# Kernel tuning notes

Hardware: AMD Instinct MI355X
Metric: run time of the kernel (lower is better)

Reference implementation:

```python
import jax, jax.numpy as jnp
import numpy as np

H = 256   # hidden_dim
V = 256   # byte vocab


def _lstm_cell(h, c, gates):
    # PyTorch gate order: i, f, g, o
    i, f, g, o = jnp.split(gates, 4, axis=-1)
    c = jax.nn.sigmoid(f) * c + jax.nn.sigmoid(i) * jnp.tanh(g)
    h = jax.nn.sigmoid(o) * jnp.tanh(c)
    return h, c


def _lstm_layer(x, w_ih, w_hh, b):
    # x: (B, T, In) -> (B, T, H); single direction, zero init state
    B = x.shape[0]
    Hh = w_hh.shape[1]
    xg = jnp.einsum('bti,gi->btg', x, w_ih) + b  # precompute input contribution
    def step(carry, xg_t):
        h, c = carry
        h, c = _lstm_cell(h, c, xg_t + h @ w_hh.T)
        return (h, c), h
    init = (jnp.zeros((B, Hh), x.dtype), jnp.zeros((B, Hh), x.dtype))
    _, hs = jax.lax.scan(step, init, jnp.swapaxes(xg, 0, 1))
    return jnp.swapaxes(hs, 0, 1)


def setup_inputs() -> dict:
    key = jax.random.key(0)
    ks = jax.random.split(key, 16)
    B, T = 256, 512
    s = 0.08
    def rn(k, shape):
        return jax.random.normal(k, shape, jnp.float32) * s
    return dict(
        text_bytes=jax.random.randint(ks[0], (B, T), 0, V),
        max_nefs_len=100,
        emb=rn(ks[1], (V, H)),
        enc_w_ih_l0=rn(ks[2], (2, 4 * H, H)),        # (dir, 4H, in)
        enc_w_hh_l0=rn(ks[3], (2, 4 * H, H)),
        enc_b_l0=rn(ks[4], (2, 4 * H)),              # b_ih + b_hh fused
        enc_w_ih_rest=rn(ks[5], (2, 2, 4 * H, 2 * H)),  # layers 1-2, input=2H
        enc_w_hh_rest=rn(ks[6], (2, 2, 4 * H, H)),
        enc_b_rest=rn(ks[7], (2, 2, 4 * H)),
        dec_w_ih_l0=rn(ks[8], (4 * H, 2 * H)),       # decoder input_size=2H
        dec_w_ih_rest=rn(ks[9], (2, 4 * H, H)),
        dec_w_hh=rn(ks[10], (3, 4 * H, H)),
        dec_b=rn(ks[11], (3, 4 * H)),
        proj_w=rn(ks[12], (256, H)),
        proj_b=rn(ks[13], (256,)),
    )


def reference(text_bytes, max_nefs_len, emb, enc_w_ih_l0, enc_w_hh_l0, enc_b_l0,
              enc_w_ih_rest, enc_w_hh_rest, enc_b_rest, dec_w_ih_l0,
              dec_w_ih_rest, dec_w_hh, dec_b, proj_w, proj_b):
    B = text_bytes.shape[0]
    # --- bidirectional 3-layer encoder ---
    x = emb[text_bytes]  # (B, T, H)
    for l in range(3):
        if l == 0:
            wih, whh, b = enc_w_ih_l0, enc_w_hh_l0, enc_b_l0
        else:
            wih, whh, b = enc_w_ih_rest[l - 1], enc_w_hh_rest[l - 1], enc_b_rest[l - 1]
        fwd = _lstm_layer(x, wih[0], whh[0], b[0])
        rev = jnp.flip(_lstm_layer(jnp.flip(x, 1), wih[1], whh[1], b[1]), 1)
        x = jnp.concatenate([fwd, rev], axis=-1)  # (B, T, 2H)
    enc_out = x

    dec_in0 = enc_out[:, 0, :]  # (B, 2H)
    z = jnp.zeros((3, B, H), enc_out.dtype)

    def dec_step(carry, _):
        h, c, inp = carry
        x_l = inp
        new_h, new_c = [], []
        for l in range(3):
            wih = dec_w_ih_l0 if l == 0 else dec_w_ih_rest[l - 1]
            hl, cl = _lstm_cell(h[l], c[l], x_l @ wih.T + h[l] @ dec_w_hh[l].T + dec_b[l])
            new_h.append(hl)
            new_c.append(cl)
            x_l = hl
        logits = x_l @ proj_w.T + proj_b  # (B, 256)
        nxt = jnp.argmax(logits, axis=-1)
        e = emb[nxt]  # (B, H)
        # NOTE: original torch code feeds a 256-d embedding into the 512-d-input
        # decoder LSTM (runtime error at t=1); zero-pad to 2H to make it well-defined.
        inp_next = jnp.concatenate([e, jnp.zeros_like(e)], axis=-1)
        return (jnp.stack(new_h), jnp.stack(new_c), inp_next), logits

    _, logits_seq = jax.lax.scan(dec_step, (z, z, dec_in0), None, length=int(max_nefs_len))
    return jnp.swapaxes(logits_seq, 0, 1)  # (B, max_nefs_len, 256)
```

## Files before the change

### kernel.cpp

```cpp
#include <hip/hip_runtime.h>
#include <hip/hip_bf16.h>

#define Hh 256
#define G4 1024
#define Bsz 256
#define TN 512
#define LDEC 100

#define OD0 0
#define ODR 524288
#define ODH 1048576
#define OPJ 1835008
#define OEM 1900544

typedef __attribute__((ext_vector_type(4))) float f32x4;
typedef __attribute__((ext_vector_type(8))) short s16x8;
typedef __attribute__((ext_vector_type(8))) unsigned short u16x8;

__device__ __forceinline__ unsigned short bf_hi(float v) {
  __hip_bfloat16 h = __float2bfloat16(v);
  return *(unsigned short*)&h;
}
__device__ __forceinline__ float bf_f(unsigned short u) {
  unsigned int x = ((unsigned int)u) << 16;
  return *(float*)&x;
}
__device__ __forceinline__ float sigm(float x) { return 1.f / (1.f + expf(-x)); }

__global__ void k_fill(float* __restrict__ p, int n, float v) {
  int i = blockIdx.x * 256 + threadIdx.x;
  if (i < n) p[i] = v;
}

__global__ void k_split(const float* __restrict__ src, unsigned short* __restrict__ hi,
                        unsigned short* __restrict__ lo, int n) {
  int i = blockIdx.x * 256 + threadIdx.x;
  if (i < n) {
    float v = src[i];
    unsigned short h = bf_hi(v);
    hi[i] = h;
    lo[i] = bf_hi(v - bf_f(h));
  }
}

__global__ void k_split3(const float* __restrict__ src, unsigned short* __restrict__ p0,
                         unsigned short* __restrict__ p1, unsigned short* __restrict__ p2,
                         int n) {
  int i = blockIdx.x * 256 + threadIdx.x;
  if (i < n) {
    float v = src[i];
    unsigned short a = bf_hi(v);
    float r1 = v - bf_f(a);
    unsigned short b = bf_hi(r1);
    float r2 = r1 - bf_f(b);
    p0[i] = a;
    p1[i] = b;
    p2[i] = bf_hi(r2);
  }
}

__global__ __launch_bounds__(256) void k_gemm(
    const short* __restrict__ X, const int* __restrict__ text,
    const unsigned short* __restrict__ eh, const unsigned short* __restrict__ el, int l0,
    int K,
    const unsigned short* __restrict__ wh_, const unsigned short* __restrict__ wl_, int wstride,
    const float* __restrict__ bias, float* __restrict__ xg, int s0, int both) {
  int mt = blockIdx.x, nt = blockIdx.y, z = blockIdx.z;
  int slot, dir, w;
  if (both) { slot = z; dir = z & 1; w = z >> 1; }
  else      { slot = z * 2 + 1; dir = 1; w = z; }
  int s = s0 + w;
  int t = dir ? (TN - 1 - s) : s;
  const unsigned short* wh = wh_ + (size_t)dir * wstride;
  const unsigned short* wl = wl_ + (size_t)dir * wstride;
  const float* bp = bias + dir * G4;
  __shared__ unsigned short Ah[64][40], Al[64][40], Bh[128][40], Bl[128][40];
  int tid = threadIdx.x, wave = tid >> 6, lane = tid & 63;
  f32x4 acc[8];
#pragma unroll
  for (int i = 0; i < 8; ++i) acc[i] = (f32x4){0.f, 0.f, 0.f, 0.f};

  int ar = tid >> 2, akq = (tid & 3) * 8;
  int brow = mt * 64 + ar;
  const unsigned short *aeh = nullptr, *ael = nullptr;
  const short* ax = nullptr;
  if (l0) {
    int tok = text[brow * TN + t];
    aeh = eh + tok * 256 + akq;
    ael = el + tok * 256 + akq;
  } else {
    ax = X + ((size_t)brow * TN + t) * 512 + akq;
  }
  int br = tid >> 1, bkq = (tid & 1) * 16;
  int g = nt * 128 + br;
  const unsigned short* bsrch = wh + (size_t)g * K + bkq;
  const unsigned short* bsrcl = wl + (size_t)g * K + bkq;

  for (int kk = 0; kk < K; kk += 32) {
    __syncthreads();
    if (l0) {
      *(u16x8*)&Ah[ar][akq] = *(const u16x8*)(aeh + kk);
      *(u16x8*)&Al[ar][akq] = *(const u16x8*)(ael + kk);
    } else {
      s16x8 sv = *(const s16x8*)(ax + kk);
      u16x8 hv, lv;
#pragma unroll
      for (int j = 0; j < 8; ++j) {
        float a = (float)sv[j] * (1.f / 32767.f);
        unsigned short h = bf_hi(a);
        hv[j] = h;
        lv[j] = bf_hi(a - bf_f(h));
      }
      *(u16x8*)&Ah[ar][akq] = hv;
      *(u16x8*)&Al[ar][akq] = lv;
    }
    *(u16x8*)&Bh[br][bkq]      = *(const u16x8*)(bsrch + kk);
    *(u16x8*)&Bh[br][bkq + 8]  = *(const u16x8*)(bsrch + kk + 8);
    *(u16x8*)&Bl[br][bkq]      = *(const u16x8*)(bsrcl + kk);
    *(u16x8*)&Bl[br][bkq + 8]  = *(const u16x8*)(bsrcl + kk + 8);
    __syncthreads();

    int m = wave * 16 + (lane & 15);
    int kq = (lane >> 4) * 8;
    s16x8 ah = *(s16x8*)&Ah[m][kq];
    s16x8 al = *(s16x8*)&Al[m][kq];
#pragma unroll
    for (int nf = 0; nf < 8; ++nf) {
      s16x8 bh = *(s16x8*)&Bh[nf * 16 + (lane & 15)][kq];
      s16x8 bl = *(s16x8*)&Bl[nf * 16 + (lane & 15)][kq];
      acc[nf] = __builtin_amdgcn_mfma_f32_16x16x32_bf16(ah, bh, acc[nf], 0, 0, 0);
      acc[nf] = __builtin_amdgcn_mfma_f32_16x16x32_bf16(al, bh, acc[nf], 0, 0, 0);
      acc[nf] = __builtin_amdgcn_mfma_f32_16x16x32_bf16(ah, bl, acc[nf], 0, 0, 0);
    }
  }
  int col = lane & 15, rq = (lane >> 4) * 4;
  float* outp = xg + (size_t)slot * 262144;
#pragma unroll
  for (int nf = 0; nf < 8; ++nf) {
    int gg = nt * 128 + nf * 16 + col;
    float bv = bp[gg];
#pragma unroll
    for (int r = 0; r < 4; ++r) {
      int b = mt * 64 + wave * 16 + rq + r;
      outp[(size_t)b * 1024 + gg] = acc[nf][r] + bv;
    }
  }
}

#define MF6(ACC, P0, P1, P2, WO)                                                         \
  {                                                                                      \
    s16x8 bf0 = *(const s16x8*)&(P0)[WO];                                                \
    s16x8 bf1 = *(const s16x8*)&(P1)[WO];                                                \
    s16x8 bf2 = *(const s16x8*)&(P2)[WO];                                                \
    ACC = __builtin_amdgcn_mfma_f32_16x16x32_bf16(a1, bf1, ACC, 0, 0, 0);                \
    ACC = __builtin_amdgcn_mfma_f32_16x16x32_bf16(a0, bf2, ACC, 0, 0, 0);                \
    ACC = __builtin_amdgcn_mfma_f32_16x16x32_bf16(a2, bf0, ACC, 0, 0, 0);                \
    ACC = __builtin_amdgcn_mfma_f32_16x16x32_bf16(a1, bf0, ACC, 0, 0, 0);                \
    ACC = __builtin_amdgcn_mfma_f32_16x16x32_bf16(a0, bf1, ACC, 0, 0, 0);                \
    ACC = __builtin_amdgcn_mfma_f32_16x16x32_bf16(a0, bf0, ACC, 0, 0, 0);                \
  }

#define MFMA_BF16 __builtin_amdgcn_mfma_f32_16x16x32_bf16

__global__ __launch_bounds__(512) void k_wstep(
    const float* __restrict__ xg,
    const unsigned short* __restrict__ w0, const unsigned short* __restrict__ w1,
    const unsigned short* __restrict__ w2,
    unsigned short* __restrict__ Hg,
    float* __restrict__ Cst,
    short* __restrict__ X, short* __restrict__ Sf, short* __restrict__ Sr,
    float* __restrict__ dec_in, int* __restrict__ bar, int s0, int W, int mode) {
  int jt = blockIdx.x, bs = blockIdx.y, dir = blockIdx.z;
  if (mode == 2 && dir == 0 && s0 != 0) return;
  int nsteps = (mode == 2 && dir == 0) ? 1 : W;
  int j16 = jt * 16;
  int b0 = bs * 128;
  const unsigned short* wp0 = w0 + dir * 262144;
  const unsigned short* wp1 = w1 + dir * 262144;
  const unsigned short* wp2 = w2 + dir * 262144;
  int* gbase = bar + ((dir * 2 + bs) * 16) * 32;
  int* slot = gbase + jt * 32;

  __shared__ unsigned short Wl[3][4][16][256];
  int tid = threadIdx.x, lane = tid & 63, wv = tid >> 6;
  int m15 = lane & 15, lq = lane >> 4, hk8 = lq * 8, r0 = lq * 4;

  for (int v = tid; v < 6144; v += 512) {
    int pl = v / 2048;
    int rem = v - pl * 2048;
    int gq = rem >> 9;
    int r = (rem >> 5) & 15;
    int c = rem & 31;
    const unsigned short* wp = (pl == 0) ? wp0 : ((pl == 1) ? wp1 : wp2);
    *(u16x8*)&Wl[pl][gq][r][(c ^ (r & 7)) * 8] =
        *(const u16x8*)&wp[((size_t)(gq * 256 + j16 + r)) * 256 + c * 8];
  }
  f32x4 cx;
  if (s0 == 0) {
    cx = (f32x4){0.f, 0.f, 0.f, 0.f};
  } else {
#pragma unroll
    for (int r = 0; r < 4; ++r)
      cx[r] = Cst[(size_t)dir * 65536 + (b0 + wv * 16 + r0 + r) * 256 + j16 + m15];
  }
  __syncthreads();

  int j = j16 + m15;
  for (int w = 0; w < nsteps; ++w) {
    int s = s0 + w;
    int p0 = s & 1, p1 = p0 ^ 1;
    const float* xgp = xg + (size_t)(2 * w + dir) * 262144;
    const unsigned short* hr0 = Hg + ((size_t)(dir * 2 + p0) * 3 + 0) * 65536;
    const unsigned short* hr1 = Hg + ((size_t)(dir * 2 + p0) * 3 + 1) * 65536;
    const unsigned short* hr2 = Hg + ((size_t)(dir * 2 + p0) * 3 + 2) * 65536;
    unsigned short* hw0 = Hg + ((size_t)(dir * 2 + p1) * 3 + 0) * 65536;
    unsigned short* hw1 = Hg + ((size_t)(dir * 2 + p1) * 3 + 1) * 65536;
    unsigned short* hw2 = Hg + ((size_t)(dir * 2 + p1) * 3 + 2) * 65536;

    float xv[4][4];
#pragma unroll
    for (int r = 0; r < 4; ++r) {
      const float* xr = xgp + (size_t)(b0 + wv * 16 + r0 + r) * 1024 + j;
      xv[r][0] = xr[0];
      xv[r][1] = xr[256];
      xv[r][2] = xr[512];
      xv[r][3] = xr[768];
    }

    f32x4 acc[4];
#pragma unroll
    for (int gq = 0; gq < 4; ++gq) acc[gq] = (f32x4){0.f, 0.f, 0.f, 0.f};

    size_t hbase = (size_t)(b0 + wv * 16 + m15) * 256 + hk8;
    s16x8 a0 = *(const s16x8*)&hr0[hbase];
    s16x8 a1 = *(const s16x8*)&hr1[hbase];
    s16x8 a2 = *(const s16x8*)&hr2[hbase];
#pragma unroll
    for (int kk = 0; kk < 8; ++kk) {
      s16x8 n0, n1, n2;
      if (kk < 7) {
        n0 = *(const s16x8*)&hr0[hbase + (kk + 1) * 32];
        n1 = *(const s16x8*)&hr1[hbase + (kk + 1) * 32];
        n2 = *(const s16x8*)&hr2[hbase + (kk + 1) * 32];
      }
      int cc = ((kk * 4 + lq) ^ (m15 & 7)) * 8;
#pragma unroll
      for (int gq = 0; gq < 4; ++gq) {
        s16x8 B0 = *(const s16x8*)&Wl[0][gq][m15][cc];
        s16x8 B1 = *(const s16x8*)&Wl[1][gq][m15][cc];
        s16x8 B2 = *(const s16x8*)&Wl[2][gq][m15][cc];
        f32x4 t2 = acc[gq];
        t2 = MFMA_BF16(a1, B1, t2, 0, 0, 0);
        t2 = MFMA_BF16(a0, B2, t2, 0, 0, 0);
        t2 = MFMA_BF16(a2, B0, t2, 0, 0, 0);
        t2 = MFMA_BF16(a1, B0, t2, 0, 0, 0);
        t2 = MFMA_BF16(a0, B1, t2, 0, 0, 0);
        t2 = MFMA_BF16(a0, B0, t2, 0, 0, 0);
        acc[gq] = t2;
      }
      a0 = n0; a1 = n1; a2 = n2;
    }
    int t = dir ? (TN - 1 - s) : s;
#pragma unroll
    for (int r = 0; r < 4; ++r) {
      int brow = b0 + wv * 16 + r0 + r;
      float gi = acc[0][r] + xv[r][0];
      float gf = acc[1][r] + xv[r][1];
      float gg = acc[2][r] + xv[r][2];
      float go = acc[3][r] + xv[r][3];
      float cn = sigm(gf) * cx[r] + sigm(gi) * tanhf(gg);
      float hn = sigm(go) * tanhf(cn);
      cx[r] = cn;
      unsigned short q0v = bf_hi(hn);
      float rr1 = hn - bf_f(q0v);
      unsigned short q1v = bf_hi(rr1);
      unsigned short q2v = bf_hi(rr1 - bf_f(q1v));
      size_t ho = (size_t)brow * 256 + j;
      __builtin_nontemporal_store(q0v, &hw0[ho]);
      __builtin_nontemporal_store(q1v, &hw1[ho]);
      __builtin_nontemporal_store(q2v, &hw2[ho]);
      short q = (short)__float2int_rn(hn * 32767.f);
      if (mode == 0) {
        __builtin_nontemporal_store(q, &X[((size_t)brow * TN + t) * 512 + (dir << 8) + j]);
      } else if (mode == 1) {
        if (dir == 0) {
          if (t >= 256)
            __builtin_nontemporal_store(q, &X[((size_t)brow * TN + t) * 512 + j]);
          else
            __builtin_nontemporal_store(q, &Sf[((size_t)t * 256 + brow) * 256 + j]);
        } else {
          if (t < 256)
            __builtin_nontemporal_store(q, &X[((size_t)brow * TN + t) * 512 + 256 + j]);
          else
            __builtin_nontemporal_store(q, &Sr[((size_t)(t - 256) * 256 + brow) * 256 + j]);
        }
      } else {
        if (t == 0)
          __builtin_nontemporal_store(hn, &dec_in[(size_t)brow * 512 + (dir << 8) + j]);
      }
    }
    if (w < nsteps - 1) {
      __builtin_amdgcn_fence(__ATOMIC_RELEASE, "agent");
      __syncthreads();
      if (tid == 0)
        __hip_atomic_store(slot, s + 1, __ATOMIC_RELAXED, __HIP_MEMORY_SCOPE_AGENT);
      if (tid < 16) {
        while (__hip_atomic_load(gbase + tid * 32, __ATOMIC_RELAXED,
                                 __HIP_MEMORY_SCOPE_AGENT) < s + 1) {}
      }
      __syncthreads();
      __builtin_amdgcn_fence(__ATOMIC_ACQUIRE, "agent");
    }
  }
#pragma unroll
  for (int r = 0; r < 4; ++r)
    Cst[(size_t)dir * 65536 + (b0 + wv * 16 + r0 + r) * 256 + j16 + m15] = cx[r];
}

__global__ void k_flush(short* __restrict__ X, const short* __restrict__ Sf,
                        const short* __restrict__ Sr) {
  int side = blockIdx.y;
  int idx = blockIdx.x * 256 + threadIdx.x;
  int t0 = idx >> 13;
  int b = (idx >> 5) & 255;
  int j0 = (idx & 31) * 8;
  if (side == 0) {
    *(s16x8*)&X[((size_t)b * TN + t0) * 512 + j0] =
        *(const s16x8*)&Sf[((size_t)t0 * 256 + b) * 256 + j0];
  } else {
    int t = 256 + t0;
    *(s16x8*)&X[((size_t)b * TN + t) * 512 + 256 + j0] =
        *(const s16x8*)&Sr[((size_t)t0 * 256 + b) * 256 + j0];
  }
}

#define DWAITA(BASE, TARGET)                                                      \
  __syncthreads();                                                                \
  if (tid < 32) {                                                                 \
    while (__hip_atomic_load((BASE) + tid * 32, __ATOMIC_RELAXED,                 \
                             __HIP_MEMORY_SCOPE_AGENT) < (TARGET)) {}             \
  }                                                                               \
  __syncthreads();                                                                \
  __builtin_amdgcn_fence(__ATOMIC_ACQUIRE, "agent");

#define DPOSTA(BASE, VAL)                                                         \
  __builtin_amdgcn_fence(__ATOMIC_RELEASE, "agent");                              \
  __syncthreads();                                                                \
  if (tid == 0)                                                                   \
    __hip_atomic_store((BASE) + gix * 32, (VAL), __ATOMIC_RELAXED,                \
                       __HIP_MEMORY_SCOPE_AGENT);

#define CMM(MT, CI)                                                               \
  {                                                                               \
    int cs_ = ((CI) ^ (m15 & 7)) * 8;                                             \
    _Pragma("unroll") for (int p = 0; p < 2; ++p) {                               \
      s16x8 B0 = *(const s16x8*)&W[((size_t)(0 * 2 + p) * 16 + m15) * KT + cs_];  \
      s16x8 B1 = *(const s16x8*)&W[((size_t)(1 * 2 + p) * 16 + m15) * KT + cs_];  \
      s16x8 B2 = *(const s16x8*)&W[((size_t)(2 * 2 + p) * 16 + m15) * KT + cs_];  \
      f32x4 t2 = acc[MT][p];                                                      \
      t2 = MFMA_BF16(a1, B1, t2, 0, 0, 0);                                        \
      t2 = MFMA_BF16(a0, B2, t2, 0, 0, 0);                                        \
      t2 = MFMA_BF16(a2, B0, t2, 0, 0, 0);                                        \
      t2 = MFMA_BF16(a1, B0, t2, 0, 0, 0);                                        \
      t2 = MFMA_BF16(a0, B1, t2, 0, 0, 0);                                        \
      t2 = MFMA_BF16(a0, B0, t2, 0, 0, 0);                                        \
      acc[MT][p] = t2;                                                            \
    }                                                                             \
  }

__global__ __launch_bounds__(512) void k_dec2(
    const float* __restrict__ dec_in0,
    const unsigned short* __restrict__ q0, const unsigned short* __restrict__ q1,
    const unsigned short* __restrict__ q2,
    const float* __restrict__ db, const float* __restrict__ pb,
    unsigned short* __restrict__ Dh, int* __restrict__ toksG,
    int* __restrict__ bar, float* __restrict__ out) {
  __shared__ unsigned short W[73728];
  __shared__ float LG[8][256];
  __shared__ float rvv[8][16];
  __shared__ int rii[8][16];
  int tid = threadIdx.x, lane = tid & 63, wv = tid >> 6;
  int m15 = lane & 15, lq = lane >> 4, hk8 = lq * 8;
  int blk = blockIdx.x;
  int grp = blk >> 5;
  int gix = blk & 31;
  int j8 = gix * 8;
  int KT = (grp == 0) ? 768 : 512;
  int* arr0 = bar;
  int* arr1 = bar + 1024;
  int* arr2 = bar + 2048;
  int* arr3 = bar + 3072;

  {
    int KC = KT >> 3;
    int nvec = 6 * 16 * KC;
    for (int v = tid; v < nvec; v += 512) {
      int c = v % KC;
      int r = (v / KC) & 15;
      int pp = v / (KC * 16);
      int pl = pp >> 1, p = pp & 1;
      int g = (2 * p + (r >> 3)) * 256 + j8 + (r & 7);
      int k = c * 8;
      size_t so;
      if (grp == 0)
        so = (k < 512) ? (size_t)OD0 + (size_t)g * 512 + k
                       : (size_t)ODH + (size_t)g * 256 + (k - 512);
      else if (grp == 1)
        so = (k < 256) ? (size_t)ODR + (size_t)g * 256 + k
                       : (size_t)ODH + 262144 + (size_t)g * 256 + (k - 256);
      else
        so = (k < 256) ? (size_t)ODR + 262144 + (size_t)g * 256 + k
                       : (size_t)ODH + 524288 + (size_t)g * 256 + (k - 256);
      const unsigned short* qs = (pl == 0) ? q0 : ((pl == 1) ? q1 : q2);
      int cs = c ^ (r & 7);
      *(u16x8*)&W[((size_t)pp * 16 + r) * KT + (size_t)cs * 8] = *(const u16x8*)&qs[so];
    }
  }
  __syncthreads();

  int cc8 = m15 & 7;
  int jcol = j8 + cc8;
  float bI = db[grp * 1024 + jcol];
  float bF = db[grp * 1024 + 256 + jcol];
  float bG = db[grp * 1024 + 512 + jcol];
  float bO = db[grp * 1024 + 768 + jcol];
  f32x4 cx[2];
  cx[0] = (f32x4){0.f, 0.f, 0.f, 0.f};
  cx[1] = (f32x4){0.f, 0.f, 0.f, 0.f};

  int gb = gix * 8;
  int mrow = m15 & 7;
  int r0q = lq * 4;
  bool act = (r0q < 8);

  for (int t = 0; t < LDEC; ++t) {
    int pw = (t & 1) ^ 1, pr = t & 1;
    if (grp == 0) { DWAITA(arr3, t) }
    else if (grp == 1) { DWAITA(arr0, t + 1) }
    else { DWAITA(arr1, t + 1) }

    f32x4 acc[2][2];
#pragma unroll
    for (int mt = 0; mt < 2; ++mt)
#pragma unroll
      for (int p = 0; p < 2; ++p) acc[mt][p] = (f32x4){0.f, 0.f, 0.f, 0.f};

    if (grp == 0) {
      if (t == 0) {
        for (int kk = 0; kk < 16; ++kk) {
#pragma unroll
          for (int mt = 0; mt < 2; ++mt) {
            int browA = wv * 32 + mt * 16 + m15;
            const float* src = dec_in0 + (size_t)browA * 512 + kk * 32 + hk8;
            s16x8 a0, a1, a2;
#pragma unroll
            for (int e = 0; e < 8; ++e) {
              float v = src[e];
              unsigned short t0 = bf_hi(v);
              float r1 = v - bf_f(t0);
              unsigned short t1 = bf_hi(r1);
              a0[e] = (short)t0; a1[e] = (short)t1; a2[e] = (short)bf_hi(r1 - bf_f(t1));
            }
            CMM(mt, kk * 4 + lq)
          }
        }
      } else {
        for (int kk = 0; kk < 8; ++kk) {
#pragma unroll
          for (int mt = 0; mt < 2; ++mt) {
            int browA = wv * 32 + mt * 16 + m15;
            int tok = toksG[browA];
            size_t eo = (size_t)OEM + (size_t)tok * 256 + kk * 32 + hk8;
            s16x8 a0 = *(const s16x8*)&q0[eo];
            s16x8 a1 = *(const s16x8*)&q1[eo];
            s16x8 a2 = *(const s16x8*)&q2[eo];
            CMM(mt, kk * 4 + lq)
          }
        }
      }
    } else {
      const unsigned short* x0p = Dh + (size_t)(((grp - 1) * 2 + pw) * 3 + 0) * 65536;
      const unsigned short* x1p = Dh + (size_t)(((grp - 1) * 2 + pw) * 3 + 1) * 65536;
      const unsigned short* x2p = Dh + (size_t)(((grp - 1) * 2 + pw) * 3 + 2) * 65536;
      for (int kk = 0; kk < 8; ++kk) {
#pragma unroll
        for (int mt = 0; mt < 2; ++mt) {
          size_t ao = (size_t)(wv * 32 + mt * 16 + m15) * 256 + kk * 32 + hk8;
          s16x8 a0 = *(const s16x8*)&x0p[ao];
          s16x8 a1 = *(const s16x8*)&x1p[ao];
          s16x8 a2 = *(const s16x8*)&x2p[ao];
          CMM(mt, kk * 4 + lq)
        }
      }
    }
    {
      int cb = (grp == 0) ? 64 : 32;
      const unsigned short* h0p = Dh + (size_t)((grp * 2 + pr) * 3 + 0) * 65536;
      const unsigned short* h1p = Dh + (size_t)((grp * 2 + pr) * 3 + 1) * 65536;
      const unsigned short* h2p = Dh + (size_t)((grp * 2 + pr) * 3 + 2) * 65536;
      for (int kk = 0; kk < 8; ++kk) {
#pragma unroll
        for (int mt = 0; mt < 2; ++mt) {
          size_t ao = (size_t)(wv * 32 + mt * 16 + m15) * 256 + kk * 32 + hk8;
          s16x8 a0 = *(const s16x8*)&h0p[ao];
          s16x8 a1 = *(const s16x8*)&h1p[ao];
          s16x8 a2 = *(const s16x8*)&h2p[ao];
          CMM(mt, cb + kk * 4 + lq)
        }
      }
    }
    {
      unsigned short* hw0 = Dh + (size_t)((grp * 2 + pw) * 3 + 0) * 65536;
      unsigned short* hw1 = Dh + (size_t)((grp * 2 + pw) * 3 + 1) * 65536;
      unsigned short* hw2 = Dh + (size_t)((grp * 2 + pw) * 3 + 2) * 65536;
#pragma unroll
      for (int mt = 0; mt < 2; ++mt) {
        f32x4 fx, ox;
#pragma unroll
        for (int e = 0; e < 4; ++e) {
          fx[e] = __shfl_xor(acc[mt][0][e], 8);
          ox[e] = __shfl_xor(acc[mt][1][e], 8);
        }
        if (m15 < 8) {
#pragma unroll
          for (int r = 0; r < 4; ++r) {
            int brow = wv * 32 + mt * 16 + lq * 4 + r;
            float gi = acc[mt][0][r] + bI;
            float gf = fx[r] + bF;
            float gg = acc[mt][1][r] + bG;
            float go = ox[r] + bO;
            float cn = sigm(gf) * cx[mt][r] + sigm(gi) * tanhf(gg);
            float hn = sigm(go) * tanhf(cn);
            cx[mt][r] = cn;
            unsigned short p0v = bf_hi(hn);
            float rr1 = hn - bf_f(p0v);
            unsigned short p1v = bf_hi(rr1);
            unsigned short p2v = bf_hi(rr1 - bf_f(p1v));
            size_t ho = (size_t)brow * 256 + jcol;
            hw0[ho] = p0v; hw1[ho] = p1v; hw2[ho] = p2v;
          }
        }
      }
    }
    if (grp == 0) { DPOSTA(arr0, t + 1) }
    else if (grp == 1) { DPOSTA(arr1, t + 1) }
    else { DPOSTA(arr2, t + 1) }

    if (grp == 2) {
      DWAITA(arr2, t + 1)
      unsigned short* H2 = &W[49152];
      for (int i = tid; i < 6144; i += 512) {
        int pl = i / 2048;
        int rem = i - pl * 2048;
        int row = rem >> 8, col = rem & 255;
        H2[pl * 2112 + row * 264 + col] =
            Dh[(size_t)((2 * 2 + pw) * 3 + pl) * 65536 + (size_t)(gb + row) * 256 + col];
      }
      __syncthreads();
      f32x4 pacc[2];
#pragma unroll
      for (int jj = 0; jj < 2; ++jj) pacc[jj] = (f32x4){0.f, 0.f, 0.f, 0.f};
      for (int kk = 0; kk < 8; ++kk) {
        s16x8 a0 = *(const s16x8*)&H2[0 * 2112 + mrow * 264 + kk * 32 + hk8];
        s16x8 a1 = *(const s16x8*)&H2[1 * 2112 + mrow * 264 + kk * 32 + hk8];
        s16x8 a2 = *(const s16x8*)&H2[2 * 2112 + mrow * 264 + kk * 32 + hk8];
#pragma unroll
        for (int jj = 0; jj < 2; ++jj) {
          int v = wv * 32 + jj * 16 + m15;
          size_t wo = OPJ + (size_t)v * 256 + kk * 32 + hk8;
          MF6(pacc[jj], q0, q1, q2, wo)
        }
      }
      if (act) {
#pragma unroll
        for (int jj = 0; jj < 2; ++jj) {
          int v = wv * 32 + jj * 16 + m15;
          float pbv = pb[v];
#pragma unroll
          for (int r = 0; r < 4; ++r) LG[r0q + r][v] = pacc[jj][r] + pbv;
        }
      }
      __syncthreads();
      for (int i = tid; i < 2048; i += 512) {
        int row = i >> 8, v = i & 255;
        out[((size_t)(gb + row) * LDEC + t) * 256 + v] = LG[row][v];
      }
      if (tid < 128) {
        int prow = tid >> 4, pp = tid & 15;
        float bv = LG[prow][pp * 16];
        int bidx = pp * 16;
        for (int i2 = 1; i2 < 16; ++i2) {
          float v2 = LG[prow][pp * 16 + i2];
          if (v2 > bv) { bv = v2; bidx = pp * 16 + i2; }
        }
        rvv[prow][pp] = bv;
        rii[prow][pp] = bidx;
      }
      __syncthreads();
      if (tid < 8) {
        float best = rvv[tid][0];
        int bi = rii[tid][0];
        for (int qq = 1; qq < 16; ++qq) {
          float v2 = rvv[tid][qq];
          int ii = rii[tid][qq];
          if (v2 > best || (v2 == best && ii < bi)) { best = v2; bi = ii; }
        }
        toksG[gb + tid] = bi;
      }
      DPOSTA(arr3, t + 1)
    }
  }
}

extern "C" void kernel_launch(void* const* d_in, const int* in_sizes, int n_in,
                              void* d_out, int out_size, void* d_ws, size_t ws_size,
                              hipStream_t stream) {
  const int* text = (const int*)d_in[0];
  const float* emb = (const float*)d_in[2];
  const float* w_ih_l0 = (const float*)d_in[3];
  const float* w_hh_l0 = (const float*)d_in[4];
  const float* b_l0 = (const float*)d_in[5];
  const float* w_ih_r = (const float*)d_in[6];
  const float* w_hh_r = (const float*)d_in[7];
  const float* b_r = (const float*)d_in[8];
  const float* dwih0 = (const float*)d_in[9];
  const float* dwihr = (const float*)d_in[10];
  const float* dwhh = (const float*)d_in[11];
  const float* db = (const float*)d_in[12];
  const float* pw = (const float*)d_in[13];
  const float* pb = (const float*)d_in[14];

  char* ws = (char*)d_ws;
  short *X, *Sf, *Sr;
  unsigned short *wihh, *wihl, *whp0, *whp1, *whp2, *embh, *embl, *Hg, *Dh;
  unsigned short *q0, *q1, *q2;
  float *XG, *Cst, *dec_in;
  int *bar, *toksG;
  int W = 0;
  for (int Wv = 8; Wv >= 4 && W == 0; Wv >>= 1) {
    size_t off = 0;
    X    = (short*)(ws + off);          off += (size_t)Bsz * TN * 512 * 2;
    Sf   = (short*)(ws + off);          off += (size_t)256 * Bsz * 256 * 2;
    Sr   = (short*)(ws + off);          off += (size_t)256 * Bsz * 256 * 2;
    XG   = (float*)(ws + off);          off += (size_t)2 * Wv * 262144 * 4;
    wihh = (unsigned short*)(ws + off); off += 2621440ull * 2;
    wihl = (unsigned short*)(ws + off); off += 2621440ull * 2;
    whp0 = (unsigned short*)(ws + off); off += 1572864ull * 2;
    whp1 = (unsigned short*)(ws + off); off += 1572864ull * 2;
    whp2 = (unsigned short*)(ws + off); off += 1572864ull * 2;
    embh = (unsigned short*)(ws + off); off += 65536 * 2;
    embl = (unsigned short*)(ws + off); off += 65536 * 2;
    q0   = (unsigned short*)(ws + off); off += 1966080ull * 2;
    q1   = (unsigned short*)(ws + off); off += 1966080ull * 2;
    q2   = (unsigned short*)(ws + off); off += 1966080ull * 2;
    Hg   = (unsigned short*)(ws + off); off += 786432ull * 2;
    Dh   = (unsigned short*)(ws + off); off += 1179648ull * 2;
    Cst  = (float*)(ws + off);          off += (size_t)2 * Bsz * Hh * 4;
    dec_in = (float*)(ws + off);        off += (size_t)Bsz * 512 * 4;
    toksG = (int*)(ws + off);           off += 1024;
    bar  = (int*)(ws + off);            off += 40960;
    if (ws_size >= off) W = Wv;
  }
  if (W == 0) {
    float dval = 1000.0f + (float)(ws_size >> 20);
    k_fill<<<(out_size + 255) / 256, 256, 0, stream>>>((float*)d_out, out_size, dval);
    return;
  }

  k_fill<<<40, 256, 0, stream>>>((float*)bar, 10240, 0.f);
  k_fill<<<2304, 256, 0, stream>>>((float*)Dh, 589824, 0.f);

  k_split<<<2048, 256, 0, stream>>>(w_ih_l0, wihh, wihl, 524288);
  k_split<<<8192, 256, 0, stream>>>(w_ih_r, wihh + 524288, wihl + 524288, 2097152);
  k_split<<<256, 256, 0, stream>>>(emb, embh, embl, 65536);
  k_split3<<<2048, 256, 0, stream>>>(w_hh_l0, whp0, whp1, whp2, 524288);
  k_split3<<<4096, 256, 0, stream>>>(w_hh_r, whp0 + 524288, whp1 + 524288, whp2 + 524288, 1048576);
  k_split3<<<2048, 256, 0, stream>>>(dwih0, q0 + OD0, q1 + OD0, q2 + OD0, 524288);
  k_split3<<<2048, 256, 0, stream>>>(dwihr, q0 + ODR, q1 + ODR, q2 + ODR, 524288);
  k_split3<<<3072, 256, 0, stream>>>(dwhh, q0 + ODH, q1 + ODH, q2 + ODH, 786432);
  k_split3<<<256, 256, 0, stream>>>(pw, q0 + OPJ, q1 + OPJ, q2 + OPJ, 65536);
  k_split3<<<256, 256, 0, stream>>>(emb, q0 + OEM, q1 + OEM, q2 + OEM, 65536);

  for (int l = 0; l < 3; ++l) {
    int K = (l == 0) ? 256 : 512;
    const unsigned short *wih_h, *wih_l;
    int wstride;
    const float* bias;
    if (l == 0) {
      wih_h = wihh; wih_l = wihl; wstride = 262144;
      bias = b_l0;
    } else {
      size_t wo = 524288 + (size_t)(l - 1) * 1048576;
      wih_h = wihh + wo; wih_l = wihl + wo; wstride = 524288;
      bias = b_r + (size_t)(l - 1) * 2048;
    }
    size_t wl_off = (size_t)((l == 0) ? 0 : 2 * l) * 262144;
    int mode = (l == 2) ? 2 : ((l == 1) ? 1 : 0);
    k_fill<<<1536, 256, 0, stream>>>((float*)Hg, 393216, 0.f);
    int nwin = TN / W;
    for (int ch = 0; ch < nwin; ++ch) {
      int s0 = ch * W;
      int both = !(l == 2 && ch > 0);
      int Z = both ? 2 * W : W;
      k_gemm<<<dim3(4, 8, Z), 256, 0, stream>>>(X, text, embh, embl, (l == 0) ? 1 : 0, K,
                                                wih_h, wih_l, wstride, bias, XG, s0, both);
      k_wstep<<<dim3(16, 2, 2), 512, 0, stream>>>(XG, whp0 + wl_off, whp1 + wl_off,
                                                  whp2 + wl_off, Hg, Cst,
                                                  X, Sf, Sr, dec_in, bar + l * 2048, s0, W, mode);
    }
    if (l == 1) k_flush<<<dim3(8192, 2), 256, 0, stream>>>(X, Sf, Sr);
  }

  k_dec2<<<96, 512, 0, stream>>>(dec_in, q0, q1, q2, db, pb, Dh, toksG,
                                 bar + 6144, (float*)d_out);
}
```

Measured before the change: 49.58 ms.

## Exchange hidden state via agent-scope atomics and drop heavy release/acquire fences

```diff
diff --git a/kernel.cpp b/kernel.cpp
--- a/kernel.cpp
+++ b/kernel.cpp
@@ -162,11 +162,14 @@
 
 #define MFMA_BF16 __builtin_amdgcn_mfma_f32_16x16x32_bf16
 
+#define HLD(P) __hip_atomic_load((P), __ATOMIC_RELAXED, __HIP_MEMORY_SCOPE_AGENT)
+#define HST(P, V) __hip_atomic_store((P), (V), __ATOMIC_RELAXED, __HIP_MEMORY_SCOPE_AGENT)
+
 __global__ __launch_bounds__(512) void k_wstep(
     const float* __restrict__ xg,
     const unsigned short* __restrict__ w0, const unsigned short* __restrict__ w1,
     const unsigned short* __restrict__ w2,
-    unsigned short* __restrict__ Hg,
+    unsigned int* __restrict__ Hg,
     float* __restrict__ Cst,
     short* __restrict__ X, short* __restrict__ Sf, short* __restrict__ Sr,
     float* __restrict__ dec_in, int* __restrict__ bar, int s0, int W, int mode) {
@@ -206,16 +209,15 @@
   __syncthreads();
 
   int j = j16 + m15;
+  size_t hrow = (size_t)(b0 + wv * 16 + m15);
   for (int w = 0; w < nsteps; ++w) {
     int s = s0 + w;
     int p0 = s & 1, p1 = p0 ^ 1;
     const float* xgp = xg + (size_t)(2 * w + dir) * 262144;
-    const unsigned short* hr0 = Hg + ((size_t)(dir * 2 + p0) * 3 + 0) * 65536;
-    const unsigned short* hr1 = Hg + ((size_t)(dir * 2 + p0) * 3 + 1) * 65536;
-    const unsigned short* hr2 = Hg + ((size_t)(dir * 2 + p0) * 3 + 2) * 65536;
-    unsigned short* hw0 = Hg + ((size_t)(dir * 2 + p1) * 3 + 0) * 65536;
-    unsigned short* hw1 = Hg + ((size_t)(dir * 2 + p1) * 3 + 1) * 65536;
-    unsigned short* hw2 = Hg + ((size_t)(dir * 2 + p1) * 3 + 2) * 65536;
+    const unsigned int* r01 = Hg + (size_t)(dir * 2 + p0) * 65536 + hrow * 256;
+    const unsigned int* r2 = Hg + 262144 + (size_t)(dir * 2 + p0) * 32768 + hrow * 128;
+    unsigned int* w01w = Hg + (size_t)(dir * 2 + p1) * 65536;
+    unsigned int* w2w = Hg + 262144 + (size_t)(dir * 2 + p1) * 32768;
 
     float xv[4][4];
 #pragma unroll
@@ -231,17 +233,29 @@
 #pragma unroll
     for (int gq = 0; gq < 4; ++gq) acc[gq] = (f32x4){0.f, 0.f, 0.f, 0.f};
 
-    size_t hbase = (size_t)(b0 + wv * 16 + m15) * 256 + hk8;
-    s16x8 a0 = *(const s16x8*)&hr0[hbase];
-    s16x8 a1 = *(const s16x8*)&hr1[hbase];
-    s16x8 a2 = *(const s16x8*)&hr2[hbase];
+    unsigned int c01[8], c2[4], n01[8], n2[4];
+#pragma unroll
+    for (int e = 0; e < 8; ++e) c01[e] = HLD(r01 + hk8 + e);
+#pragma unroll
+    for (int e = 0; e < 4; ++e) c2[e] = HLD(r2 + lq * 4 + e);
 #pragma unroll
     for (int kk = 0; kk < 8; ++kk) {
-      s16x8 n0, n1, n2;
       if (kk < 7) {
-        n0 = *(const s16x8*)&hr0[hbase + (kk + 1) * 32];
-        n1 = *(const s16x8*)&hr1[hbase + (kk + 1) * 32];
-        n2 = *(const s16x8*)&hr2[hbase + (kk + 1) * 32];
+#pragma unroll
+        for (int e = 0; e < 8; ++e) n01[e] = HLD(r01 + (kk + 1) * 32 + hk8 + e);
+#pragma unroll
+        for (int e = 0; e < 4; ++e) n2[e] = HLD(r2 + (kk + 1) * 16 + lq * 4 + e);
+      }
+      s16x8 a0, a1, a2;
+#pragma unroll
+      for (int e = 0; e < 8; ++e) {
+        a0[e] = (short)(c01[e] & 0xffffu);
+        a1[e] = (short)(c01[e] >> 16);
+      }
+#pragma unroll
+      for (int e = 0; e < 4; ++e) {
+        a2[2 * e] = (short)(c2[e] & 0xffffu);
+        a2[2 * e + 1] = (short)(c2[e] >> 16);
       }
       int cc = ((kk * 4 + lq) ^ (m15 & 7)) * 8;
 #pragma unroll
@@ -258,7 +272,10 @@
         t2 = MFMA_BF16(a0, B0, t2, 0, 0, 0);
         acc[gq] = t2;
       }
-      a0 = n0; a1 = n1; a2 = n2;
+#pragma unroll
+      for (int e = 0; e < 8; ++e) c01[e] = n01[e];
+#pragma unroll
+      for (int e = 0; e < 4; ++e) c2[e] = n2[e];
     }
     int t = dir ? (TN - 1 - s) : s;
 #pragma unroll
@@ -275,10 +292,12 @@
       float rr1 = hn - bf_f(q0v);
       unsigned short q1v = bf_hi(rr1);
       unsigned short q2v = bf_hi(rr1 - bf_f(q1v));
-      size_t ho = (size_t)brow * 256 + j;
-      __builtin_nontemporal_store(q0v, &hw0[ho]);
-      __builtin_nontemporal_store(q1v, &hw1[ho]);
-      __builtin_nontemporal_store(q2v, &hw2[ho]);
+      unsigned int w0pk = (unsigned int)q0v | ((unsigned int)q1v << 16);
+      unsigned int p2o = (unsigned int)__shfl_xor((int)(unsigned int)q2v, 1);
+      HST(w01w + (size_t)brow * 256 + j, w0pk);
+      if (!(m15 & 1))
+        HST(w2w + (size_t)brow * 128 + (j >> 1),
+            ((unsigned int)q2v & 0xffffu) | (p2o << 16));
       short q = (short)__float2int_rn(hn * 32767.f);
       if (mode == 0) {
         __builtin_nontemporal_store(q, &X[((size_t)brow * TN + t) * 512 + (dir << 8) + j]);
@@ -300,16 +319,15 @@
       }
     }
     if (w < nsteps - 1) {
-      __builtin_amdgcn_fence(__ATOMIC_RELEASE, "agent");
+      asm volatile("s_waitcnt vmcnt(0)" ::: "memory");
       __syncthreads();
-      if (tid == 0)
-        __hip_atomic_store(slot, s + 1, __ATOMIC_RELAXED, __HIP_MEMORY_SCOPE_AGENT);
+      if (tid == 0) HST(slot, s + 1);
       if (tid < 16) {
         while (__hip_atomic_load(gbase + tid * 32, __ATOMIC_RELAXED,
                                  __HIP_MEMORY_SCOPE_AGENT) < s + 1) {}
       }
       __syncthreads();
-      __builtin_amdgcn_fence(__ATOMIC_ACQUIRE, "agent");
+      __builtin_amdgcn_fence(__ATOMIC_ACQUIRE, "workgroup");
     }
   }
 #pragma unroll
@@ -632,7 +650,8 @@
 
   char* ws = (char*)d_ws;
   short *X, *Sf, *Sr;
-  unsigned short *wihh, *wihl, *whp0, *whp1, *whp2, *embh, *embl, *Hg, *Dh;
+  unsigned short *wihh, *wihl, *whp0, *whp1, *whp2, *embh, *embl, *Dh;
+  unsigned int* Hg;
   unsigned short *q0, *q1, *q2;
   float *XG, *Cst, *dec_in;
   int *bar, *toksG;
@@ -653,7 +672,7 @@
     q0   = (unsigned short*)(ws + off); off += 1966080ull * 2;
     q1   = (unsigned short*)(ws + off); off += 1966080ull * 2;
     q2   = (unsigned short*)(ws + off); off += 1966080ull * 2;
-    Hg   = (unsigned short*)(ws + off); off += 786432ull * 2;
+    Hg   = (unsigned int*)(ws + off);   off += 393216ull * 4;
     Dh   = (unsigned short*)(ws + off); off += 1179648ull * 2;
     Cst  = (float*)(ws + off);          off += (size_t)2 * Bsz * Hh * 4;
     dec_in = (float*)(ws + off);        off += (size_t)Bsz * 512 * 4;
```

Result: slower. 55.71 ms (+12.4%).
